# Kernel optimization log

Measured on AMD Instinct MI355X. Metric: run time of the kernel, lower is better.

The kernel has to match this reference:

```python
import jax, jax.numpy as jnp
import numpy as np

NEG_BIG = -1e10


def setup_inputs() -> dict:
    key = jax.random.key(0)
    k1, k2, k3 = jax.random.split(key, 3)
    B, C, S, H = 4, 32, 64, 256
    inputs = jax.random.normal(k1, (B, C, S, H), dtype=jnp.float32)
    mask = jnp.ones((B, C, S), dtype=jnp.float32)
    att_self = jax.random.uniform(k2, (B, C, S), dtype=jnp.float32)
    W = jax.random.normal(k3, (H, H), dtype=jnp.float32) * (1.0 / np.sqrt(H))
    return {"inputs": inputs, "mask": mask, "att_self": att_self, "W": W}


def reference(inputs, mask, att_self, W):
    # inputs: [B, C, S, H]; mask, att_self: [B, C, S]; W: [H, H] (linear1, no bias)
    # linear1(inputs2): x @ W^T applied to the query-side copy
    proj = jnp.einsum('bish,gh->bisg', inputs, W)          # [B, C, S, H]
    # scores[b,i,j,s,t] = proj[b,i,s,:] . inputs[b,j,t,:]
    scores = jnp.einsum('bish,bjth->bijst', proj, inputs)  # [B, C, C, S, S]
    # additive mask depends on (j, t) only (key side), broadcast over i and s
    scores = scores + (1.0 - mask)[:, None, :, None, :] * NEG_BIG
    # torch code computes softmax then overwrites with sigmoid -> sigmoid is effective
    att = jax.nn.sigmoid(scores)                            # [B, C, C, S, S]
    ctx = jnp.einsum('bijst,bjth->bijsh', att, inputs)      # [B, C, C, S, H]
    # selfatt weights over s (query sentence tokens), indexed by i
    fused = jnp.einsum('bis,bijsh->bijh', att_self, ctx)    # [B, C, C, H]
    return (fused, att)
```

## Files before the change

### kernel.cpp

```cpp
#include <hip/hip_runtime.h>
#include <hip/hip_bf16.h>

typedef __bf16 bf16x8 __attribute__((ext_vector_type(8)));
typedef float  f32x4  __attribute__((ext_vector_type(4)));

#define NEG_BIG (-1e10f)

constexpr int FUSED_N = 4 * 32 * 32 * 256;


__device__ __forceinline__ int swz16(int row, int g) {
    return (row * 16 + (g ^ (row & 15))) * 8;
}
__device__ __forceinline__ int swzp(int row, int g) {
    return (row * 32 + (g ^ row)) * 8;
}

__device__ __forceinline__ void async_ld16(const void* g, void* l) {
    __builtin_amdgcn_global_load_lds(
        (const __attribute__((address_space(1))) void*)g,
        (__attribute__((address_space(3))) void*)l, 16, 0, 0);
}

__global__ __launch_bounds__(256) void convw_kernel(
    const float* __restrict__ W, __bf16* __restrict__ Wh, __bf16* __restrict__ Wl) {
    int idx = blockIdx.x * 256 + threadIdx.x;
    float4 v = ((const float4*)W)[idx];
    float f[4] = {v.x, v.y, v.z, v.w};
    union { __bf16 b[4]; uint2 u; } H, L;
#pragma unroll
    for (int k = 0; k < 4; ++k) {
        __bf16 h = (__bf16)f[k];
        H.b[k] = h;
        L.b[k] = (__bf16)(f[k] - (float)h);
    }
    *(uint2*)&Wh[idx * 4] = H.u;
    *(uint2*)&Wl[idx * 4] = L.u;
}

__global__ __launch_bounds__(256, 2) void prep_kernel(
    const float* __restrict__ Xf,
    const __bf16* __restrict__ Wh, const __bf16* __restrict__ Wl,
    __bf16* __restrict__ XhG, __bf16* __restrict__ XlG,
    __bf16* __restrict__ Ph, __bf16* __restrict__ Pl) {
    __shared__ __align__(16) __bf16 sXh[16 * 256];
    __shared__ __align__(16) __bf16 sXl[16 * 256];
    const int tid = threadIdx.x, rb = blockIdx.x;

#pragma unroll
    for (int it = 0; it < 2; ++it) {
        int idx = it * 256 + tid;
        int row = idx >> 5, g = idx & 31;
        const float* p = Xf + (rb * 16 + row) * 256 + g * 8;
        float4 v0 = *(const float4*)p;
        float4 v1 = *(const float4*)(p + 4);
        float f[8] = {v0.x, v0.y, v0.z, v0.w, v1.x, v1.y, v1.z, v1.w};
        union { __bf16 b[8]; uint4 u; } H, L;
#pragma unroll
        for (int k = 0; k < 8; ++k) {
            __bf16 h = (__bf16)f[k];
            H.b[k] = h;
            L.b[k] = (__bf16)(f[k] - (float)h);
        }
        int go = (rb * 16 + row) * 256 + g * 8;
        *(uint4*)&XhG[go] = H.u;
        *(uint4*)&XlG[go] = L.u;
        int o = swzp(row, g);
        *(uint4*)&sXh[o] = H.u;
        *(uint4*)&sXl[o] = L.u;
    }
    __syncthreads();

    const int lane = tid & 63, wave = tid >> 6, m = lane & 15, quad = lane >> 4;
    bf16x8 Ah[8], Al[8];
#pragma unroll
    for (int k0 = 0; k0 < 8; ++k0) {
        int o = swzp(m, k0 * 4 + quad);
        Ah[k0] = *(const bf16x8*)&sXh[o];
        Al[k0] = *(const bf16x8*)&sXl[o];
    }
    f32x4 acc[4];
    const f32x4 z = {0.f, 0.f, 0.f, 0.f};
#pragma unroll
    for (int n = 0; n < 4; ++n) acc[n] = z;
#pragma unroll
    for (int k0 = 0; k0 < 8; ++k0) {
#pragma unroll
        for (int n = 0; n < 4; ++n) {
            const int gcol = wave * 64 + n * 16 + m;
            const int wo = gcol * 256 + k0 * 32 + quad * 8;
            bf16x8 bh = *(const bf16x8*)&Wh[wo];
            bf16x8 bl = *(const bf16x8*)&Wl[wo];
            acc[n] = __builtin_amdgcn_mfma_f32_16x16x32_bf16(Ah[k0], bh, acc[n], 0, 0, 0);
            acc[n] = __builtin_amdgcn_mfma_f32_16x16x32_bf16(Ah[k0], bl, acc[n], 0, 0, 0);
            acc[n] = __builtin_amdgcn_mfma_f32_16x16x32_bf16(Al[k0], bh, acc[n], 0, 0, 0);
        }
    }
#pragma unroll
    for (int n = 0; n < 4; ++n)
#pragma unroll
        for (int r = 0; r < 4; ++r) {
            int row = rb * 16 + quad * 4 + r;
            int col = wave * 64 + n * 16 + m;
            float v = acc[n][r];
            __bf16 h = (__bf16)v;
            Ph[row * 256 + col] = h;
            Pl[row * 256 + col] = (__bf16)(v - (float)h);
        }
}

__global__ __launch_bounds__(256, 4) void main_kernel(
    const float* __restrict__ Xf, const float* __restrict__ maskf,
    const float* __restrict__ aselff,
    const __bf16* __restrict__ XhG, const __bf16* __restrict__ XlG,
    const __bf16* __restrict__ Ph, const __bf16* __restrict__ Pl,
    float* __restrict__ out) {
    __shared__ __align__(16) __bf16 sXh[64 * 128];
    __shared__ __align__(16) __bf16 sXl[64 * 128];
    __shared__ float sWpart[4 * 64];
    __shared__ float s_w[64];
    const int tid = threadIdx.x;
    const int jp = blockIdx.x & 15;
    const int i = (blockIdx.x >> 4) & 31;
    const int b = blockIdx.x >> 9;
    const int lane = tid & 63, wave = tid >> 6, m = lane & 15, quad = lane >> 4;
    const int xb0 = (b * 32 + jp * 2) * 16384;
    const int xb1 = xb0 + 16384;

    auto stage = [&](int xbase, int kc) {
#pragma unroll
        for (int it = 0; it < 4; ++it) {
            const int ii = wave * 4 + it;
            const int row = ii * 4 + quad;
            const int g = m ^ (row & 15);
            const int go = xbase + row * 256 + kc * 128 + g * 8;
            async_ld16(&XhG[go], &sXh[ii * 512]);
            async_ld16(&XlG[go], &sXl[ii * 512]);
        }
    };

    stage(xb0, 0);

    const int prow = ((b * 32 + i) * 64 + wave * 16 + m) * 256;
    bf16x8 Ah[8], Al[8];
#pragma unroll
    for (int k0 = 0; k0 < 8; ++k0) {
        Ah[k0] = *(const bf16x8*)&Ph[prow + k0 * 32 + quad * 8];
        Al[k0] = *(const bf16x8*)&Pl[prow + k0 * 32 + quad * 8];
    }
    const float4 aself4 = *(const float4*)&aselff[(b * 32 + i) * 64 + wave * 16 + quad * 4];
    float madd[2][4];
#pragma unroll
    for (int jt = 0; jt < 2; ++jt) {
        const float* mrow = maskf + (b * 32 + jp * 2 + jt) * 64;
#pragma unroll
        for (int n = 0; n < 4; ++n) madd[jt][n] = (1.0f - mrow[n * 16 + m]) * NEG_BIG;
    }

    const f32x4 z = {0.f, 0.f, 0.f, 0.f};
    f32x4 acc[4];

    auto mfma_chunk = [&](int kc) {
#pragma unroll
        for (int k0 = 0; k0 < 4; ++k0) {
            const int ak = kc * 4 + k0;
#pragma unroll
            for (int n = 0; n < 4; ++n) {
                const int bo = swz16(n * 16 + m, k0 * 4 + quad);
                bf16x8 bh = *(const bf16x8*)&sXh[bo];
                bf16x8 bl = *(const bf16x8*)&sXl[bo];
                acc[n] = __builtin_amdgcn_mfma_f32_16x16x32_bf16(Ah[ak], bh, acc[n], 0, 0, 0);
                acc[n] = __builtin_amdgcn_mfma_f32_16x16x32_bf16(Ah[ak], bl, acc[n], 0, 0, 0);
                acc[n] = __builtin_amdgcn_mfma_f32_16x16x32_bf16(Al[ak], bh, acc[n], 0, 0, 0);
            }
        }
    };

    auto epilogue = [&](int jt, int xbase, bool prefetch, int xnext) {
        const int j = jp * 2 + jt;
        float* outA = out + FUSED_N + ((size_t)((b * 32 + i) * 32 + j)) * 4096;
        float part[4];
#pragma unroll
        for (int n = 0; n < 4; ++n) {
            const int t = n * 16 + m;
            float p = 0.f;
#pragma unroll
            for (int r = 0; r < 4; ++r) {
                const int s = wave * 16 + quad * 4 + r;
                float x = acc[n][r] + madd[jt][n];
                float a = 1.0f / (1.0f + __expf(-x));
                outA[s * 64 + t] = a;
                p += ((const float*)&aself4)[r] * a;
            }
            part[n] = p;
        }
#pragma unroll
        for (int n = 0; n < 4; ++n) {
            part[n] += __shfl_xor(part[n], 16, 64);
            part[n] += __shfl_xor(part[n], 32, 64);
        }
        if (quad == 0) {
#pragma unroll
            for (int n = 0; n < 4; ++n) sWpart[wave * 64 + n * 16 + m] = part[n];
        }
        __syncthreads();
        if (prefetch) stage(xnext, 0);
        if (tid < 64)
            s_w[tid] = sWpart[tid] + sWpart[64 + tid] + sWpart[128 + tid] + sWpart[192 + tid];
        __syncthreads();
        const float* Xg = Xf + xbase;
        float acf = 0.f;
#pragma unroll 8
        for (int t = 0; t < 64; ++t) acf += s_w[t] * Xg[t * 256 + tid];
        out[((size_t)((b * 32 + i) * 32 + j)) * 256 + tid] = acf;
    };

#pragma unroll
    for (int n = 0; n < 4; ++n) acc[n] = z;
    __syncthreads();
    mfma_chunk(0);
    __syncthreads();
    stage(xb0, 1);
    __syncthreads();
    mfma_chunk(1);
    epilogue(0, xb0, true, xb1);

#pragma unroll
    for (int n = 0; n < 4; ++n) acc[n] = z;
    mfma_chunk(0);
    __syncthreads();
    stage(xb1, 1);
    __syncthreads();
    mfma_chunk(1);
    epilogue(1, xb1, false, 0);
}

extern "C" void kernel_launch(void* const* d_in, const int* in_sizes, int n_in,
                              void* d_out, int out_size, void* d_ws, size_t ws_size,
                              hipStream_t stream) {
    const float* X     = (const float*)d_in[0];
    const float* mask  = (const float*)d_in[1];
    const float* aself = (const float*)d_in[2];
    const float* W     = (const float*)d_in[3];
    float* out = (float*)d_out;

    __bf16* ws = (__bf16*)d_ws;
    const size_t NX = 2097152, NW = 65536;
    __bf16* Xh = ws;
    __bf16* Xl = Xh + NX;
    __bf16* Ph = Xl + NX;
    __bf16* Pl = Ph + NX;
    __bf16* Wh = Pl + NX;
    __bf16* Wl = Wh + NW;

    convw_kernel<<<dim3(64), dim3(256), 0, stream>>>(W, Wh, Wl);
    prep_kernel<<<dim3(512), dim3(256), 0, stream>>>(X, Wh, Wl, Xh, Xl, Ph, Pl);
    main_kernel<<<dim3(2048), dim3(256), 0, stream>>>(
        X, mask, aself, Xh, Xl, Ph, Pl, out);
}
```

Baseline: 176.8 us.

## Restructure main kernel: P tile in LDS, one key sentence per wave

```diff
diff --git a/kernel.cpp b/kernel.cpp
--- a/kernel.cpp
+++ b/kernel.cpp
@@ -8,18 +8,15 @@
 
 constexpr int FUSED_N = 4 * 32 * 32 * 256;
 
-
-__device__ __forceinline__ int swz16(int row, int g) {
-    return (row * 16 + (g ^ (row & 15))) * 8;
-}
-__device__ __forceinline__ int swzp(int row, int g) {
-    return (row * 32 + (g ^ row)) * 8;
-}
 
 __device__ __forceinline__ void async_ld16(const void* g, void* l) {
     __builtin_amdgcn_global_load_lds(
         (const __attribute__((address_space(1))) void*)g,
         (__attribute__((address_space(3))) void*)l, 16, 0, 0);
+}
+
+__device__ __forceinline__ int swzp(int row, int g) {
+    return (row * 32 + (g ^ row)) * 8;
 }
 
 __global__ __launch_bounds__(256) void convw_kernel(
@@ -109,130 +106,125 @@
         }
 }
 
-__global__ __launch_bounds__(256, 4) void main_kernel(
+__global__ __launch_bounds__(256, 2) void main_kernel(
     const float* __restrict__ Xf, const float* __restrict__ maskf,
     const float* __restrict__ aselff,
     const __bf16* __restrict__ XhG, const __bf16* __restrict__ XlG,
-    const __bf16* __restrict__ Ph, const __bf16* __restrict__ Pl,
+    const __bf16* __restrict__ PhG, const __bf16* __restrict__ PlG,
     float* __restrict__ out) {
-    __shared__ __align__(16) __bf16 sXh[64 * 128];
-    __shared__ __align__(16) __bf16 sXl[64 * 128];
-    __shared__ float sWpart[4 * 64];
-    __shared__ float s_w[64];
+    __shared__ __align__(16) __bf16 sPh[64 * 256];
+    __shared__ __align__(16) __bf16 sPl[64 * 256];
+    __shared__ float sW[4][64];
     const int tid = threadIdx.x;
-    const int jp = blockIdx.x & 15;
-    const int i = (blockIdx.x >> 4) & 31;
-    const int b = blockIdx.x >> 9;
+    const int jq = blockIdx.x & 3;
+    const int i  = (blockIdx.x >> 2) & 31;
+    const int b  = blockIdx.x >> 7;
     const int lane = tid & 63, wave = tid >> 6, m = lane & 15, quad = lane >> 4;
-    const int xb0 = (b * 32 + jp * 2) * 16384;
-    const int xb1 = xb0 + 16384;
-
-    auto stage = [&](int xbase, int kc) {
-#pragma unroll
-        for (int it = 0; it < 4; ++it) {
-            const int ii = wave * 4 + it;
-            const int row = ii * 4 + quad;
-            const int g = m ^ (row & 15);
-            const int go = xbase + row * 256 + kc * 128 + g * 8;
-            async_ld16(&XhG[go], &sXh[ii * 512]);
-            async_ld16(&XlG[go], &sXl[ii * 512]);
-        }
-    };
-
-    stage(xb0, 0);
-
-    const int prow = ((b * 32 + i) * 64 + wave * 16 + m) * 256;
-    bf16x8 Ah[8], Al[8];
-#pragma unroll
-    for (int k0 = 0; k0 < 8; ++k0) {
-        Ah[k0] = *(const bf16x8*)&Ph[prow + k0 * 32 + quad * 8];
-        Al[k0] = *(const bf16x8*)&Pl[prow + k0 * 32 + quad * 8];
-    }
-    const float4 aself4 = *(const float4*)&aselff[(b * 32 + i) * 64 + wave * 16 + quad * 4];
-    float madd[2][4];
-#pragma unroll
+
+    const int pbase = (b * 32 + i) * 16384;
+    {
+        const int rowhalf = lane >> 5;
+        const int gslot = lane & 31;
+#pragma unroll
+        for (int it = 0; it < 8; ++it) {
+            const int insti = wave * 8 + it;
+            const int row = insti * 2 + rowhalf;
+            const int g = gslot ^ (row & 15);
+            const int src = pbase + row * 256 + g * 8;
+            async_ld16(&PhG[src], &sPh[insti * 512]);
+            async_ld16(&PlG[src], &sPl[insti * 512]);
+        }
+    }
+
+    const float* ap = aselff + (b * 32 + i) * 64;
+    float4 asv[4];
+#pragma unroll
+    for (int rg = 0; rg < 4; ++rg)
+        asv[rg] = *(const float4*)&ap[rg * 16 + quad * 4];
+
+    __syncthreads();
+
     for (int jt = 0; jt < 2; ++jt) {
-        const float* mrow = maskf + (b * 32 + jp * 2 + jt) * 64;
-#pragma unroll
-        for (int n = 0; n < 4; ++n) madd[jt][n] = (1.0f - mrow[n * 16 + m]) * NEG_BIG;
-    }
-
-    const f32x4 z = {0.f, 0.f, 0.f, 0.f};
-    f32x4 acc[4];
-
-    auto mfma_chunk = [&](int kc) {
-#pragma unroll
-        for (int k0 = 0; k0 < 4; ++k0) {
-            const int ak = kc * 4 + k0;
-#pragma unroll
-            for (int n = 0; n < 4; ++n) {
-                const int bo = swz16(n * 16 + m, k0 * 4 + quad);
-                bf16x8 bh = *(const bf16x8*)&sXh[bo];
-                bf16x8 bl = *(const bf16x8*)&sXl[bo];
-                acc[n] = __builtin_amdgcn_mfma_f32_16x16x32_bf16(Ah[ak], bh, acc[n], 0, 0, 0);
-                acc[n] = __builtin_amdgcn_mfma_f32_16x16x32_bf16(Ah[ak], bl, acc[n], 0, 0, 0);
-                acc[n] = __builtin_amdgcn_mfma_f32_16x16x32_bf16(Al[ak], bh, acc[n], 0, 0, 0);
+        const int j = jq * 8 + jt * 4 + wave;
+        const int xb = (b * 32 + j) * 16384;
+
+        f32x4 acc[4][4];
+        const f32x4 z = {0.f, 0.f, 0.f, 0.f};
+#pragma unroll
+        for (int rg = 0; rg < 4; ++rg)
+#pragma unroll
+            for (int ng = 0; ng < 4; ++ng) acc[rg][ng] = z;
+
+#pragma unroll
+        for (int k0 = 0; k0 < 8; ++k0) {
+            bf16x8 Bh[4], Bl[4];
+#pragma unroll
+            for (int ng = 0; ng < 4; ++ng) {
+                const int bo = xb + (ng * 16 + m) * 256 + k0 * 32 + quad * 8;
+                Bh[ng] = *(const bf16x8*)&XhG[bo];
+                Bl[ng] = *(const bf16x8*)&XlG[bo];
             }
-        }
-    };
-
-    auto epilogue = [&](int jt, int xbase, bool prefetch, int xnext) {
-        const int j = jp * 2 + jt;
+            bf16x8 Ahk[4], Alk[4];
+#pragma unroll
+            for (int rg = 0; rg < 4; ++rg) {
+                const int o = (rg * 16 + m) * 256 + (((k0 * 4 + quad) ^ m)) * 8;
+                Ahk[rg] = *(const bf16x8*)&sPh[o];
+                Alk[rg] = *(const bf16x8*)&sPl[o];
+            }
+#pragma unroll
+            for (int rg = 0; rg < 4; ++rg)
+#pragma unroll
+                for (int ng = 0; ng < 4; ++ng) {
+                    acc[rg][ng] = __builtin_amdgcn_mfma_f32_16x16x32_bf16(Ahk[rg], Bh[ng], acc[rg][ng], 0, 0, 0);
+                    acc[rg][ng] = __builtin_amdgcn_mfma_f32_16x16x32_bf16(Ahk[rg], Bl[ng], acc[rg][ng], 0, 0, 0);
+                    acc[rg][ng] = __builtin_amdgcn_mfma_f32_16x16x32_bf16(Alk[rg], Bh[ng], acc[rg][ng], 0, 0, 0);
+                }
+        }
+
+        const float* mrow = maskf + (b * 32 + j) * 64;
+        float madd[4];
+#pragma unroll
+        for (int ng = 0; ng < 4; ++ng)
+            madd[ng] = (1.0f - mrow[ng * 16 + m]) * NEG_BIG;
+
+        float part[4] = {0.f, 0.f, 0.f, 0.f};
         float* outA = out + FUSED_N + ((size_t)((b * 32 + i) * 32 + j)) * 4096;
-        float part[4];
-#pragma unroll
-        for (int n = 0; n < 4; ++n) {
-            const int t = n * 16 + m;
-            float p = 0.f;
+#pragma unroll
+        for (int rg = 0; rg < 4; ++rg)
 #pragma unroll
             for (int r = 0; r < 4; ++r) {
-                const int s = wave * 16 + quad * 4 + r;
-                float x = acc[n][r] + madd[jt][n];
-                float a = 1.0f / (1.0f + __expf(-x));
-                outA[s * 64 + t] = a;
-                p += ((const float*)&aself4)[r] * a;
+                const int s = rg * 16 + quad * 4 + r;
+                const float as_ = ((const float*)&asv[rg])[r];
+#pragma unroll
+                for (int ng = 0; ng < 4; ++ng) {
+                    float x = acc[rg][ng][r] + madd[ng];
+                    float a = 1.0f / (1.0f + __expf(-x));
+                    outA[s * 64 + ng * 16 + m] = a;
+                    part[ng] += as_ * a;
+                }
             }
-            part[n] = p;
-        }
-#pragma unroll
-        for (int n = 0; n < 4; ++n) {
-            part[n] += __shfl_xor(part[n], 16, 64);
-            part[n] += __shfl_xor(part[n], 32, 64);
+#pragma unroll
+        for (int ng = 0; ng < 4; ++ng) {
+            part[ng] += __shfl_xor(part[ng], 16, 64);
+            part[ng] += __shfl_xor(part[ng], 32, 64);
         }
         if (quad == 0) {
 #pragma unroll
-            for (int n = 0; n < 4; ++n) sWpart[wave * 64 + n * 16 + m] = part[n];
-        }
-        __syncthreads();
-        if (prefetch) stage(xnext, 0);
-        if (tid < 64)
-            s_w[tid] = sWpart[tid] + sWpart[64 + tid] + sWpart[128 + tid] + sWpart[192 + tid];
-        __syncthreads();
-        const float* Xg = Xf + xbase;
-        float acf = 0.f;
+            for (int ng = 0; ng < 4; ++ng) sW[wave][ng * 16 + m] = part[ng];
+        }
+        const float* Xg = Xf + xb;
+        float4 acf = {0.f, 0.f, 0.f, 0.f};
 #pragma unroll 8
-        for (int t = 0; t < 64; ++t) acf += s_w[t] * Xg[t * 256 + tid];
-        out[((size_t)((b * 32 + i) * 32 + j)) * 256 + tid] = acf;
-    };
-
-#pragma unroll
-    for (int n = 0; n < 4; ++n) acc[n] = z;
-    __syncthreads();
-    mfma_chunk(0);
-    __syncthreads();
-    stage(xb0, 1);
-    __syncthreads();
-    mfma_chunk(1);
-    epilogue(0, xb0, true, xb1);
-
-#pragma unroll
-    for (int n = 0; n < 4; ++n) acc[n] = z;
-    mfma_chunk(0);
-    __syncthreads();
-    stage(xb1, 1);
-    __syncthreads();
-    mfma_chunk(1);
-    epilogue(1, xb1, false, 0);
+        for (int t = 0; t < 64; ++t) {
+            const float wv = sW[wave][t];
+            float4 xv = *(const float4*)&Xg[t * 256 + lane * 4];
+            acf.x += wv * xv.x;
+            acf.y += wv * xv.y;
+            acf.z += wv * xv.z;
+            acf.w += wv * xv.w;
+        }
+        *(float4*)&out[((size_t)((b * 32 + i) * 32 + j)) * 256 + lane * 4] = acf;
+    }
 }
 
 extern "C" void kernel_launch(void* const* d_in, const int* in_sizes, int n_in,
@@ -255,6 +247,6 @@
 
     convw_kernel<<<dim3(64), dim3(256), 0, stream>>>(W, Wh, Wl);
     prep_kernel<<<dim3(512), dim3(256), 0, stream>>>(X, Wh, Wl, Xh, Xl, Ph, Pl);
-    main_kernel<<<dim3(2048), dim3(256), 0, stream>>>(
+    main_kernel<<<dim3(512), dim3(256), 0, stream>>>(
         X, mask, aself, Xh, Xl, Ph, Pl, out);
 }
```

Measured after the change: 149.3 us. 1.18x faster.
